# Kernel optimization log

Measured on AMD Instinct MI355X. Metric: run time of the kernel, lower is better.

## Reference

```python
import jax, jax.numpy as jnp
import numpy as np

B, IN, HID, OUT, E, K = 16384, 512, 1024, 512, 16, 4


def setup_inputs() -> dict:
    key = jax.random.key(0)
    k0, k1, k2, k3 = jax.random.split(key, 4)
    return {
        "x": jax.random.normal(k0, (B, IN), jnp.float32),
        "w_gate": jax.random.normal(k1, (IN, E), jnp.float32) * 0.02,
        "w1": jax.random.normal(k2, (E, IN, HID), jnp.float32) * (1.0 / np.sqrt(IN)),
        "b1": jnp.zeros((E, HID), jnp.float32),
        "w2": jax.random.normal(k3, (E, HID, OUT), jnp.float32) * (1.0 / np.sqrt(HID)),
        "b2": jnp.zeros((E, OUT), jnp.float32),
    }


def _top_k_gating(x, w_gate):
    # Eval-mode (no noise) noisy_top_k_gating: logits -> top-(k+1) -> softmax over top-k
    logits = x @ w_gate  # [B, E]
    m = min(K + 1, E)
    top_logits, top_idx = jax.lax.top_k(logits, m)  # [B, m]
    tk_logits = top_logits[:, :K]                    # [B, K]
    tk_idx = top_idx[:, :K]                          # [B, K] int32
    tk_gates = jax.nn.softmax(tk_logits, axis=1)     # softmax over the k selected
    rows = jnp.arange(logits.shape[0])[:, None]
    gates = jnp.zeros_like(logits).at[rows, tk_idx].set(tk_gates)  # sparse [B, E]
    return gates


def reference(x, w_gate, w1, b1, w2, b2):
    # Gating
    gates = _top_k_gating(x, w_gate)  # [B, E], zero for non-selected experts
    # Dispatch/combine: output[b] = sum_e gates[b,e] * MLP_e(x[b]).
    # Torch code only evaluates experts on selected rows; since gates are exactly
    # zero elsewhere, the dense weighted sum below computes identical math.
    y = jnp.zeros((x.shape[0], w2.shape[2]), x.dtype)
    for e in range(E):  # fixed small expert count; each iter is one grouped GEMM pair
        h = jax.nn.relu(x @ w1[e] + b1[e])                 # [B, HID]
        o = jax.nn.softmax(h @ w2[e] + b2[e], axis=1)      # expert MLP ends in Softmax(dim=1)
        y = y + gates[:, e:e + 1] * o
    return y
```

## Files before the change

kernel.cpp:

```cpp
#include <hip/hip_runtime.h>
#include <hip/hip_fp16.h>

typedef _Float16 f16;
typedef _Float16 f16x8 __attribute__((ext_vector_type(8)));
typedef float f32x4 __attribute__((ext_vector_type(4)));

#define MFMA(a,b,c) __builtin_amdgcn_mfma_f32_16x16x32_f16((a),(b),(c),0,0,0)

#define BAR() do { \
  asm volatile("s_waitcnt lgkmcnt(0)" ::: "memory"); \
  __builtin_amdgcn_sched_barrier(0); \
  __builtin_amdgcn_s_barrier(); \
  __builtin_amdgcn_sched_barrier(0); \
} while (0)


__global__ void k_cvt_w1(const float* __restrict__ w1, f16* __restrict__ w1fr) {
  int fid = blockIdx.x * 4 + (threadIdx.x >> 6);
  int l = threadIdx.x & 63;
  int e = fid >> 10, n0 = (fid >> 4) & 63, kc = fid & 15;
  int kbase = kc * 32 + (l >> 4) * 8;
  int col = n0 * 16 + (l & 15);
  const float* src = w1 + ((size_t)e * 512 + kbase) * 1024 + col;
  f16x8 o;
  #pragma unroll
  for (int i = 0; i < 8; i++) o[i] = (f16)src[(size_t)i * 1024];
  *(f16x8*)(w1fr + (size_t)fid * 512 + l * 8) = o;
}

__global__ void k_cvt_w2(const float* __restrict__ w2, f16* __restrict__ w2fr) {
  int fid = blockIdx.x * 4 + (threadIdx.x >> 6);
  int l = threadIdx.x & 63;
  int e = fid >> 10, n0 = (fid >> 5) & 31, kc = fid & 31;
  int kbase = kc * 32 + (l >> 4) * 8;
  int col = n0 * 16 + (l & 15);
  const float* src = w2 + ((size_t)e * 1024 + kbase) * 512 + col;
  f16x8 o;
  #pragma unroll
  for (int i = 0; i < 8; i++) o[i] = (f16)src[(size_t)i * 512];
  *(f16x8*)(w2fr + (size_t)fid * 512 + l * 8) = o;
}

__global__ void k_gate(const float* __restrict__ x, const float* __restrict__ wg,
                       int* __restrict__ tk_idx, float* __restrict__ tk_gate) {
  int w = threadIdx.x >> 6, l = threadIdx.x & 63;
  int r = blockIdx.x * 4 + w;
  float p[16];
  #pragma unroll
  for (int e = 0; e < 16; e++) p[e] = 0.f;
  const float* xr = x + (size_t)r * 512;
  #pragma unroll
  for (int t = 0; t < 8; t++) {
    float xv = xr[t * 64 + l];
    const float* wrow = wg + (t * 64 + l) * 16;
    #pragma unroll
    for (int e = 0; e < 16; e++) p[e] += xv * wrow[e];
  }
  #pragma unroll
  for (int e = 0; e < 16; e++) {
    float v = p[e];
    #pragma unroll
    for (int m = 32; m >= 1; m >>= 1) v += __shfl_xor(v, m);
    p[e] = v;
  }
  unsigned chosen = 0;
  float bv[4]; int bi[4];
  #pragma unroll
  for (int j = 0; j < 4; j++) {
    float best = -3.4e38f; int be = 0;
    #pragma unroll
    for (int e = 0; e < 16; e++) {
      bool ok = !((chosen >> e) & 1u) && (p[e] > best);
      if (ok) { best = p[e]; be = e; }
    }
    chosen |= 1u << be; bv[j] = best; bi[j] = be;
  }
  float m0 = bv[0];
  float e0 = __expf(bv[0] - m0), e1 = __expf(bv[1] - m0),
        e2 = __expf(bv[2] - m0), e3 = __expf(bv[3] - m0);
  float s = e0 + e1 + e2 + e3;
  if (l == 0) {
    *(int4*)(tk_idx + (size_t)r * 4) = make_int4(bi[0], bi[1], bi[2], bi[3]);
    *(float4*)(tk_gate + (size_t)r * 4) = make_float4(e0 / s, e1 / s, e2 / s, e3 / s);
  }
}

__global__ void k_route_count(const int* __restrict__ tk_idx, int* __restrict__ partial) {
  int e = blockIdx.x >> 6, chunk = blockIdx.x & 63;
  int t = threadIdx.x;
  int row = chunk * 256 + t;
  int4 tk = ((const int4*)tk_idx)[row];
  bool match = (tk.x == e) || (tk.y == e) || (tk.z == e) || (tk.w == e);
  unsigned long long m = __ballot(match);
  __shared__ int wc[4];
  if ((t & 63) == 0) wc[t >> 6] = (int)__popcll(m);
  __syncthreads();
  if (t == 0) partial[e * 64 + chunk] = wc[0] + wc[1] + wc[2] + wc[3];
}

__global__ void k_route_scan(const int* __restrict__ partial, int* __restrict__ chunk_base,
                             int* __restrict__ count) {
  int l = threadIdx.x;
  for (int e = 0; e < 16; e++) {
    int v = partial[e * 64 + l];
    int orig = v;
    #pragma unroll
    for (int off = 1; off < 64; off <<= 1) {
      int u = __shfl_up(v, off);
      if (l >= off) v += u;
    }
    chunk_base[e * 64 + l] = v - orig;
    if (l == 63) count[e] = v;
  }
}

__global__ void k_route_scatter(const int* __restrict__ tk_idx, const float* __restrict__ tk_gate,
                                const int* __restrict__ chunk_base, int* __restrict__ rows_pk,
                                float* __restrict__ gates_l) {
  int e = blockIdx.x >> 6, chunk = blockIdx.x & 63;
  int t = threadIdx.x, w = t >> 6, l = t & 63;
  int row = chunk * 256 + t;
  int4 tk = ((const int4*)tk_idx)[row];
  int j = (tk.x == e) ? 0 : (tk.y == e) ? 1 : (tk.z == e) ? 2 : (tk.w == e) ? 3 : -1;
  bool match = (j >= 0);
  unsigned long long m = __ballot(match);
  __shared__ int wc[4];
  if (l == 0) wc[w] = (int)__popcll(m);
  __syncthreads();
  int wbase = 0;
  #pragma unroll
  for (int i = 0; i < 4; i++) if (i < w) wbase += wc[i];
  if (match) {
    int pos = (int)__popcll(m & ((1ULL << l) - 1ULL));
    int idx = e * 16384 + chunk_base[e * 64 + chunk] + wbase + pos;
    rows_pk[idx] = row | (j << 16);
    gates_l[idx] = tk_gate[(size_t)row * 4 + j];
  }
}

__global__ void k_zero(float4* __restrict__ y4) {
  y4[blockIdx.x * 256 + threadIdx.x] = make_float4(0.f, 0.f, 0.f, 0.f);
}

__global__ __launch_bounds__(512, 4) void k_expert(
    const float* __restrict__ x, const f16* __restrict__ w1fr, const f16* __restrict__ w2fr,
    const float* __restrict__ b1, const float* __restrict__ b2,
    const int* __restrict__ count, const int* __restrict__ rows_pk,
    const float* __restrict__ gates_l, float* __restrict__ y)
{
  int p = blockIdx.x;
  int xcd = p & 7, s = p >> 3;
  int e = (xcd << 1) | (s >> 8);
  int rb = s & 255;
  int cnt = count[e];
  int mstart = rb * 64;
  if (mstart >= cnt) return;
  int nvalid = cnt - mstart; if (nvalid > 64) nvalid = 64;

  __shared__ f16 x_lds[2][64 * 136];
  __shared__ f16 h_lds[64 * 264];
  __shared__ int rowarr[64];
  __shared__ float gatearr[64];
  __shared__ float red[2][8][64];

  int t = threadIdx.x, w = t >> 6, l = t & 63;
  int lq = l >> 4, lr = l & 15;

  if (t < 64) {
    int idx = (t < nvalid) ? t : (nvalid - 1);
    int src = e * 16384 + mstart + idx;
    rowarr[t] = rows_pk[src];
    gatearr[t] = gates_l[src];
  }
  BAR();

  int srow = t >> 3, sc0 = (t & 7) * 16;
  const float* sp = x + (size_t)(rowarr[srow] & 0xFFFF) * 512 + sc0;
  char* xl0 = (char*)&x_lds[0][0];
  char* xl1 = (char*)&x_lds[1][0];
  char* hl  = (char*)h_lds;
  int xwb = srow * 272 + sc0 * 2;

  const f16x8* w1f8 = (const f16x8*)w1fr;
  const f16x8* w2f8 = (const f16x8*)w2fr;

  f32x4 acc2[4][4];
  #pragma unroll
  for (int a = 0; a < 4; a++)
    #pragma unroll
    for (int b = 0; b < 4; b++)
      #pragma unroll
      for (int q = 0; q < 4; q++) acc2[a][b][q] = 0.f;

  #pragma unroll 1
  for (int hc = 0; hc < 4; hc++) {
    {
      const float* qp = sp;
      float4 u0 = ((const float4*)qp)[0], u1 = ((const float4*)qp)[1];
      float4 u2 = ((const float4*)qp)[2], u3 = ((const float4*)qp)[3];
      f16x8 v0, v1;
      v0[0]=(f16)u0.x; v0[1]=(f16)u0.y; v0[2]=(f16)u0.z; v0[3]=(f16)u0.w;
      v0[4]=(f16)u1.x; v0[5]=(f16)u1.y; v0[6]=(f16)u1.z; v0[7]=(f16)u1.w;
      v1[0]=(f16)u2.x; v1[1]=(f16)u2.y; v1[2]=(f16)u2.z; v1[3]=(f16)u2.w;
      v1[4]=(f16)u3.x; v1[5]=(f16)u3.y; v1[6]=(f16)u3.z; v1[7]=(f16)u3.w;
      *(f16x8*)(xl0 + xwb) = v0;
      *(f16x8*)(xl0 + xwb + 16) = v1;
    }
    const f16x8* bp1h = w1f8 + ((size_t)((e * 64 + hc * 16 + w * 2) * 16)) * 64 + l;
    f16x8 ba0 = bp1h[0], ba1 = bp1h[16 * 64];
    BAR();

    f32x4 acc1[4][2];
    #pragma unroll
    for (int a = 0; a < 4; a++)
      #pragma unroll
      for (int b = 0; b < 2; b++)
        #pragma unroll
        for (int q = 0; q < 4; q++) acc1[a][b][q] = 0.f;

    #pragma unroll 1
    for (int kk = 0; kk < 4; kk++) {
      char* xbuf = (kk & 1) ? xl1 : xl0;
      char* xnxt = (kk & 1) ? xl0 : xl1;
      float4 u0, u1, u2, u3;
      if (kk < 3) {
        const float* qp = sp + (kk + 1) * 128;
        u0 = ((const float4*)qp)[0]; u1 = ((const float4*)qp)[1];
        u2 = ((const float4*)qp)[2]; u3 = ((const float4*)qp)[3];
      }
      const f16x8* bp1 = bp1h + (size_t)(kk * 4) * 64;
      #pragma unroll
      for (int k4 = 0; k4 < 4; k4++) {
        f16x8 bb0, bb1;
        if (k4 < 3) {
          bb0 = bp1[(k4 + 1) * 64];
          bb1 = bp1[16 * 64 + (k4 + 1) * 64];
        }
        f16x8 av[4];
        #pragma unroll
        for (int mf = 0; mf < 4; mf++)
          av[mf] = *(const f16x8*)(xbuf + (mf * 16 + lr) * 272 + k4 * 64 + lq * 16);
        #pragma unroll
        for (int mf = 0; mf < 4; mf++) {
          acc1[mf][0] = MFMA(av[mf], ba0, acc1[mf][0]);
          acc1[mf][1] = MFMA(av[mf], ba1, acc1[mf][1]);
        }
        if (k4 < 3) { ba0 = bb0; ba1 = bb1; }
      }
      if (kk < 3) {
        f16x8 v0, v1;
        v0[0]=(f16)u0.x; v0[1]=(f16)u0.y; v0[2]=(f16)u0.z; v0[3]=(f16)u0.w;
        v0[4]=(f16)u1.x; v0[5]=(f16)u1.y; v0[6]=(f16)u1.z; v0[7]=(f16)u1.w;
        v1[0]=(f16)u2.x; v1[1]=(f16)u2.y; v1[2]=(f16)u2.z; v1[3]=(f16)u2.w;
        v1[4]=(f16)u3.x; v1[5]=(f16)u3.y; v1[6]=(f16)u3.z; v1[7]=(f16)u3.w;
        *(f16x8*)(xnxt + xwb) = v0;
        *(f16x8*)(xnxt + xwb + 16) = v1;
        const f16x8* bpn = bp1h + (size_t)((kk + 1) * 4) * 64;
        ba0 = bpn[0]; ba1 = bpn[16 * 64];
      }
      BAR();
    }

    #pragma unroll
    for (int nf = 0; nf < 2; nf++) {
      int colc = w * 32 + nf * 16 + lr;
      float bv = b1[e * 1024 + hc * 256 + colc];
      #pragma unroll
      for (int mf = 0; mf < 4; mf++)
        #pragma unroll
        for (int q = 0; q < 4; q++) {
          int row = mf * 16 + lq * 4 + q;
          float hv = fmaxf(acc1[mf][nf][q] + bv, 0.f);
          *(f16*)(hl + row * 528 + colc * 2) = (f16)hv;
        }
    }
    const f16x8* bp2 = w2f8 + ((size_t)((e * 32 + w * 4) * 32 + hc * 8)) * 64 + l;
    f16x8 wa0 = bp2[0], wa1 = bp2[32 * 64], wa2 = bp2[64 * 64], wa3 = bp2[96 * 64];
    BAR();

    #pragma unroll 2
    for (int kc2 = 0; kc2 < 8; kc2++) {
      f16x8 wb0, wb1, wb2, wb3;
      if (kc2 < 7) {
        wb0 = bp2[(kc2 + 1) * 64];
        wb1 = bp2[32 * 64 + (kc2 + 1) * 64];
        wb2 = bp2[64 * 64 + (kc2 + 1) * 64];
        wb3 = bp2[96 * 64 + (kc2 + 1) * 64];
      }
      f16x8 av[4];
      #pragma unroll
      for (int mf = 0; mf < 4; mf++)
        av[mf] = *(const f16x8*)(hl + (mf * 16 + lr) * 528 + kc2 * 64 + lq * 16);
      #pragma unroll
      for (int mf = 0; mf < 4; mf++) {
        acc2[mf][0] = MFMA(av[mf], wa0, acc2[mf][0]);
        acc2[mf][1] = MFMA(av[mf], wa1, acc2[mf][1]);
        acc2[mf][2] = MFMA(av[mf], wa2, acc2[mf][2]);
        acc2[mf][3] = MFMA(av[mf], wa3, acc2[mf][3]);
      }
      if (kc2 < 7) { wa0 = wb0; wa1 = wb1; wa2 = wb2; wa3 = wb3; }
    }
  }

  #pragma unroll
  for (int nf = 0; nf < 4; nf++) {
    float bv = b2[e * 512 + w * 64 + nf * 16 + lr];
    #pragma unroll
    for (int mf = 0; mf < 4; mf++)
      #pragma unroll
      for (int q = 0; q < 4; q++) acc2[mf][nf][q] += bv;
  }

  float rmax[4][4];
  #pragma unroll
  for (int mf = 0; mf < 4; mf++)
    #pragma unroll
    for (int q = 0; q < 4; q++) {
      float v = acc2[mf][0][q];
      #pragma unroll
      for (int nf = 1; nf < 4; nf++) v = fmaxf(v, acc2[mf][nf][q]);
      #pragma unroll
      for (int m = 1; m < 16; m <<= 1) v = fmaxf(v, __shfl_xor(v, m));
      rmax[mf][q] = v;
    }
  if (lr == 0) {
    #pragma unroll
    for (int mf = 0; mf < 4; mf++)
      #pragma unroll
      for (int q = 0; q < 4; q++) red[0][w][mf * 16 + lq * 4 + q] = rmax[mf][q];
  }
  BAR();
  float gmax[4][4];
  #pragma unroll
  for (int mf = 0; mf < 4; mf++)
    #pragma unroll
    for (int q = 0; q < 4; q++) {
      int row = mf * 16 + lq * 4 + q;
      float v = red[0][0][row];
      #pragma unroll
      for (int ww = 1; ww < 8; ww++) v = fmaxf(v, red[0][ww][row]);
      gmax[mf][q] = v;
    }
  float psum[4][4];
  #pragma unroll
  for (int mf = 0; mf < 4; mf++)
    #pragma unroll
    for (int q = 0; q < 4; q++) psum[mf][q] = 0.f;
  #pragma unroll
  for (int mf = 0; mf < 4; mf++)
    #pragma unroll
    for (int nf = 0; nf < 4; nf++)
      #pragma unroll
      for (int q = 0; q < 4; q++) {
        float pp = __expf(acc2[mf][nf][q] - gmax[mf][q]);
        acc2[mf][nf][q] = pp;
        psum[mf][q] += pp;
      }
  #pragma unroll
  for (int mf = 0; mf < 4; mf++)
    #pragma unroll
    for (int q = 0; q < 4; q++) {
      float v = psum[mf][q];
      #pragma unroll
      for (int m = 1; m < 16; m <<= 1) v += __shfl_xor(v, m);
      psum[mf][q] = v;
    }
  if (lr == 0) {
    #pragma unroll
    for (int mf = 0; mf < 4; mf++)
      #pragma unroll
      for (int q = 0; q < 4; q++) red[1][w][mf * 16 + lq * 4 + q] = psum[mf][q];
  }
  BAR();

  #pragma unroll
  for (int mf = 0; mf < 4; mf++) {
    #pragma unroll
    for (int q = 0; q < 4; q++) {
      int row = mf * 16 + lq * 4 + q;
      if (row < nvalid) {
        float ssum = 0.f;
        #pragma unroll
        for (int ww = 0; ww < 8; ww++) ssum += red[1][ww][row];
        float sc = gatearr[row] / ssum;
        int orow = rowarr[row] & 0xFFFF;
        float* yr = y + (size_t)orow * 512 + w * 64 + lr;
        #pragma unroll
        for (int nf = 0; nf < 4; nf++) {
          atomicAdd(yr + nf * 16, acc2[mf][nf][q] * sc);
        }
      }
    }
  }
}

extern "C" void kernel_launch(void* const* d_in, const int* in_sizes, int n_in,
                              void* d_out, int out_size, void* d_ws, size_t ws_size,
                              hipStream_t stream) {
  (void)in_sizes; (void)n_in; (void)out_size; (void)ws_size;
  const float* x  = (const float*)d_in[0];
  const float* wg = (const float*)d_in[1];
  const float* w1 = (const float*)d_in[2];
  const float* b1 = (const float*)d_in[3];
  const float* w2 = (const float*)d_in[4];
  const float* b2 = (const float*)d_in[5];
  float* y = (float*)d_out;

  char* ws = (char*)d_ws;
  size_t off = 0;
  auto alloc = [&](size_t bytes) -> char* {
    char* p = ws + off;
    off += (bytes + 255) & ~(size_t)255;
    return p;
  };
  f16*   w1fr       = (f16*)  alloc((size_t)16 * 512 * 1024 * 2);
  f16*   w2fr       = (f16*)  alloc((size_t)16 * 1024 * 512 * 2);
  int*   tk_idx     = (int*)  alloc((size_t)16384 * 4 * 4);
  float* tk_gate    = (float*)alloc((size_t)16384 * 4 * 4);
  int*   rows_pk    = (int*)  alloc((size_t)16 * 16384 * 4);
  float* gates_l    = (float*)alloc((size_t)16 * 16384 * 4);
  int*   partial    = (int*)  alloc(16 * 64 * 4);
  int*   chunk_base = (int*)  alloc(16 * 64 * 4);
  int*   count      = (int*)  alloc(256);

  k_cvt_w1<<<dim3(4096), dim3(256), 0, stream>>>(w1, w1fr);
  k_cvt_w2<<<dim3(4096), dim3(256), 0, stream>>>(w2, w2fr);
  k_gate<<<dim3(4096), dim3(256), 0, stream>>>(x, wg, tk_idx, tk_gate);
  k_route_count<<<dim3(1024), dim3(256), 0, stream>>>(tk_idx, partial);
  k_route_scan<<<dim3(1), dim3(64), 0, stream>>>(partial, chunk_base, count);
  k_route_scatter<<<dim3(1024), dim3(256), 0, stream>>>(tk_idx, tk_gate, chunk_base,
                                                        rows_pk, gates_l);
  k_zero<<<dim3(8192), dim3(256), 0, stream>>>((float4*)y);
  k_expert<<<dim3(4096), dim3(512), 0, stream>>>(x, w1fr, w2fr, b1, b2,
                                                 count, rows_pk, gates_l, y);
}
```

Before: 450.0 us.

## Double expert block to 16 waves, stage full x tile in swizzled LDS

The expert kernel now uses 1024 threads (16 waves) per block, each wave owning half as many output columns in both GEMMs. The whole 64x512 x tile is loaded and converted to fp16 once into LDS with an XOR swizzle, replacing the per-hc double-buffered reload of x. The h tile also gets an XOR-swizzled layout instead of padding. This removes the repeated x reloads and LDS bank conflicts and adds more waves for latency hiding. In exchange it drops the explicit register prefetch of weights, increases LDS use to about 96KB, which may limit blocks per CU, and doubles the softmax cross-wave reduction width.

Measured after the change: 410.0 us. 8.9% less time.

```diff
diff --git a/kernel.cpp b/kernel.cpp
--- a/kernel.cpp
+++ b/kernel.cpp
@@ -142,7 +142,7 @@
   y4[blockIdx.x * 256 + threadIdx.x] = make_float4(0.f, 0.f, 0.f, 0.f);
 }
 
-__global__ __launch_bounds__(512, 4) void k_expert(
+__global__ __launch_bounds__(1024, 4) void k_expert(
     const float* __restrict__ x, const f16* __restrict__ w1fr, const f16* __restrict__ w2fr,
     const float* __restrict__ b1, const float* __restrict__ b2,
     const int* __restrict__ count, const int* __restrict__ rows_pk,
@@ -157,11 +157,11 @@
   if (mstart >= cnt) return;
   int nvalid = cnt - mstart; if (nvalid > 64) nvalid = 64;
 
-  __shared__ f16 x_lds[2][64 * 136];
-  __shared__ f16 h_lds[64 * 264];
+  __shared__ f16 x_lds[64 * 512];
+  __shared__ f16 h_lds[64 * 256];
   __shared__ int rowarr[64];
   __shared__ float gatearr[64];
-  __shared__ float red[2][8][64];
+  __shared__ float red[2][16][64];
 
   int t = threadIdx.x, w = t >> 6, l = t & 63;
   int lq = l >> 4, lr = l & 15;
@@ -174,137 +174,95 @@
   }
   BAR();
 
-  int srow = t >> 3, sc0 = (t & 7) * 16;
-  const float* sp = x + (size_t)(rowarr[srow] & 0xFFFF) * 512 + sc0;
-  char* xl0 = (char*)&x_lds[0][0];
-  char* xl1 = (char*)&x_lds[1][0];
-  char* hl  = (char*)h_lds;
-  int xwb = srow * 272 + sc0 * 2;
+  {
+    int rX = t >> 4, s0 = t & 15;
+    const float* sp = x + (size_t)(rowarr[rX] & 0xFFFF) * 512;
+    char* xb = (char*)x_lds;
+    #pragma unroll
+    for (int j = 0; j < 4; j++) {
+      int seg = s0 + j * 16;
+      const float* qp = sp + seg * 8;
+      float4 u0 = ((const float4*)qp)[0], u1 = ((const float4*)qp)[1];
+      f16x8 v;
+      v[0]=(f16)u0.x; v[1]=(f16)u0.y; v[2]=(f16)u0.z; v[3]=(f16)u0.w;
+      v[4]=(f16)u1.x; v[5]=(f16)u1.y; v[6]=(f16)u1.z; v[7]=(f16)u1.w;
+      int byte = rX * 1024 + ((seg ^ rX) & 63) * 16;
+      *(f16x8*)(xb + byte) = v;
+    }
+  }
+  BAR();
 
   const f16x8* w1f8 = (const f16x8*)w1fr;
   const f16x8* w2f8 = (const f16x8*)w2fr;
-
-  f32x4 acc2[4][4];
+  char* xb = (char*)x_lds;
+  char* hb = (char*)h_lds;
+
+  f32x4 acc2[4][2];
   #pragma unroll
   for (int a = 0; a < 4; a++)
     #pragma unroll
-    for (int b = 0; b < 4; b++)
+    for (int b = 0; b < 2; b++)
       #pragma unroll
       for (int q = 0; q < 4; q++) acc2[a][b][q] = 0.f;
 
   #pragma unroll 1
   for (int hc = 0; hc < 4; hc++) {
+    f32x4 acc1[4];
+    #pragma unroll
+    for (int a = 0; a < 4; a++)
+      #pragma unroll
+      for (int q = 0; q < 4; q++) acc1[a][q] = 0.f;
+
+    const f16x8* bp1 = w1f8 + ((size_t)((e * 64 + hc * 16 + w) * 16)) * 64 + l;
+    #pragma unroll 4
+    for (int kcg = 0; kcg < 16; kcg++) {
+      f16x8 bf = bp1[kcg * 64];
+      int seg = kcg * 4 + lq;
+      #pragma unroll
+      for (int mf = 0; mf < 4; mf++) {
+        int row = mf * 16 + lr;
+        f16x8 av = *(const f16x8*)(xb + row * 1024 + ((seg ^ row) & 63) * 16);
+        acc1[mf] = MFMA(av, bf, acc1[mf]);
+      }
+    }
+
+    BAR();
     {
-      const float* qp = sp;
-      float4 u0 = ((const float4*)qp)[0], u1 = ((const float4*)qp)[1];
-      float4 u2 = ((const float4*)qp)[2], u3 = ((const float4*)qp)[3];
-      f16x8 v0, v1;
-      v0[0]=(f16)u0.x; v0[1]=(f16)u0.y; v0[2]=(f16)u0.z; v0[3]=(f16)u0.w;
-      v0[4]=(f16)u1.x; v0[5]=(f16)u1.y; v0[6]=(f16)u1.z; v0[7]=(f16)u1.w;
-      v1[0]=(f16)u2.x; v1[1]=(f16)u2.y; v1[2]=(f16)u2.z; v1[3]=(f16)u2.w;
-      v1[4]=(f16)u3.x; v1[5]=(f16)u3.y; v1[6]=(f16)u3.z; v1[7]=(f16)u3.w;
-      *(f16x8*)(xl0 + xwb) = v0;
-      *(f16x8*)(xl0 + xwb + 16) = v1;
-    }
-    const f16x8* bp1h = w1f8 + ((size_t)((e * 64 + hc * 16 + w * 2) * 16)) * 64 + l;
-    f16x8 ba0 = bp1h[0], ba1 = bp1h[16 * 64];
-    BAR();
-
-    f32x4 acc1[4][2];
-    #pragma unroll
-    for (int a = 0; a < 4; a++)
-      #pragma unroll
-      for (int b = 0; b < 2; b++)
-        #pragma unroll
-        for (int q = 0; q < 4; q++) acc1[a][b][q] = 0.f;
-
-    #pragma unroll 1
-    for (int kk = 0; kk < 4; kk++) {
-      char* xbuf = (kk & 1) ? xl1 : xl0;
-      char* xnxt = (kk & 1) ? xl0 : xl1;
-      float4 u0, u1, u2, u3;
-      if (kk < 3) {
-        const float* qp = sp + (kk + 1) * 128;
-        u0 = ((const float4*)qp)[0]; u1 = ((const float4*)qp)[1];
-        u2 = ((const float4*)qp)[2]; u3 = ((const float4*)qp)[3];
-      }
-      const f16x8* bp1 = bp1h + (size_t)(kk * 4) * 64;
-      #pragma unroll
-      for (int k4 = 0; k4 < 4; k4++) {
-        f16x8 bb0, bb1;
-        if (k4 < 3) {
-          bb0 = bp1[(k4 + 1) * 64];
-          bb1 = bp1[16 * 64 + (k4 + 1) * 64];
-        }
-        f16x8 av[4];
-        #pragma unroll
-        for (int mf = 0; mf < 4; mf++)
-          av[mf] = *(const f16x8*)(xbuf + (mf * 16 + lr) * 272 + k4 * 64 + lq * 16);
-        #pragma unroll
-        for (int mf = 0; mf < 4; mf++) {
-          acc1[mf][0] = MFMA(av[mf], ba0, acc1[mf][0]);
-          acc1[mf][1] = MFMA(av[mf], ba1, acc1[mf][1]);
-        }
-        if (k4 < 3) { ba0 = bb0; ba1 = bb1; }
-      }
-      if (kk < 3) {
-        f16x8 v0, v1;
-        v0[0]=(f16)u0.x; v0[1]=(f16)u0.y; v0[2]=(f16)u0.z; v0[3]=(f16)u0.w;
-        v0[4]=(f16)u1.x; v0[5]=(f16)u1.y; v0[6]=(f16)u1.z; v0[7]=(f16)u1.w;
-        v1[0]=(f16)u2.x; v1[1]=(f16)u2.y; v1[2]=(f16)u2.z; v1[3]=(f16)u2.w;
-        v1[4]=(f16)u3.x; v1[5]=(f16)u3.y; v1[6]=(f16)u3.z; v1[7]=(f16)u3.w;
-        *(f16x8*)(xnxt + xwb) = v0;
-        *(f16x8*)(xnxt + xwb + 16) = v1;
-        const f16x8* bpn = bp1h + (size_t)((kk + 1) * 4) * 64;
-        ba0 = bpn[0]; ba1 = bpn[16 * 64];
-      }
-      BAR();
-    }
-
-    #pragma unroll
-    for (int nf = 0; nf < 2; nf++) {
-      int colc = w * 32 + nf * 16 + lr;
-      float bv = b1[e * 1024 + hc * 256 + colc];
+      int cc = w * 16 + lr;
+      float bv = b1[e * 1024 + hc * 256 + cc];
+      int seg = w * 2 + (lr >> 3);
       #pragma unroll
       for (int mf = 0; mf < 4; mf++)
         #pragma unroll
         for (int q = 0; q < 4; q++) {
           int row = mf * 16 + lq * 4 + q;
-          float hv = fmaxf(acc1[mf][nf][q] + bv, 0.f);
-          *(f16*)(hl + row * 528 + colc * 2) = (f16)hv;
+          float hv = fmaxf(acc1[mf][q] + bv, 0.f);
+          int byte = row * 512 + ((seg ^ row) & 31) * 16 + (lr & 7) * 2;
+          *(f16*)(hb + byte) = (f16)hv;
         }
     }
-    const f16x8* bp2 = w2f8 + ((size_t)((e * 32 + w * 4) * 32 + hc * 8)) * 64 + l;
-    f16x8 wa0 = bp2[0], wa1 = bp2[32 * 64], wa2 = bp2[64 * 64], wa3 = bp2[96 * 64];
     BAR();
 
+    const f16x8* bp2a = w2f8 + ((size_t)((e * 32 + w * 2) * 32 + hc * 8)) * 64 + l;
+    const f16x8* bp2b = bp2a + (size_t)32 * 64;
     #pragma unroll 2
     for (int kc2 = 0; kc2 < 8; kc2++) {
-      f16x8 wb0, wb1, wb2, wb3;
-      if (kc2 < 7) {
-        wb0 = bp2[(kc2 + 1) * 64];
-        wb1 = bp2[32 * 64 + (kc2 + 1) * 64];
-        wb2 = bp2[64 * 64 + (kc2 + 1) * 64];
-        wb3 = bp2[96 * 64 + (kc2 + 1) * 64];
+      f16x8 wf0 = bp2a[kc2 * 64];
+      f16x8 wf1 = bp2b[kc2 * 64];
+      int seg = kc2 * 4 + lq;
+      #pragma unroll
+      for (int mf = 0; mf < 4; mf++) {
+        int row = mf * 16 + lr;
+        f16x8 av = *(const f16x8*)(hb + row * 512 + ((seg ^ row) & 31) * 16);
+        acc2[mf][0] = MFMA(av, wf0, acc2[mf][0]);
+        acc2[mf][1] = MFMA(av, wf1, acc2[mf][1]);
       }
-      f16x8 av[4];
-      #pragma unroll
-      for (int mf = 0; mf < 4; mf++)
-        av[mf] = *(const f16x8*)(hl + (mf * 16 + lr) * 528 + kc2 * 64 + lq * 16);
-      #pragma unroll
-      for (int mf = 0; mf < 4; mf++) {
-        acc2[mf][0] = MFMA(av[mf], wa0, acc2[mf][0]);
-        acc2[mf][1] = MFMA(av[mf], wa1, acc2[mf][1]);
-        acc2[mf][2] = MFMA(av[mf], wa2, acc2[mf][2]);
-        acc2[mf][3] = MFMA(av[mf], wa3, acc2[mf][3]);
-      }
-      if (kc2 < 7) { wa0 = wb0; wa1 = wb1; wa2 = wb2; wa3 = wb3; }
-    }
-  }
-
-  #pragma unroll
-  for (int nf = 0; nf < 4; nf++) {
-    float bv = b2[e * 512 + w * 64 + nf * 16 + lr];
+    }
+  }
+
+  #pragma unroll
+  for (int nf = 0; nf < 2; nf++) {
+    float bv = b2[e * 512 + w * 32 + nf * 16 + lr];
     #pragma unroll
     for (int mf = 0; mf < 4; mf++)
       #pragma unroll
@@ -316,9 +274,7 @@
   for (int mf = 0; mf < 4; mf++)
     #pragma unroll
     for (int q = 0; q < 4; q++) {
-      float v = acc2[mf][0][q];
-      #pragma unroll
-      for (int nf = 1; nf < 4; nf++) v = fmaxf(v, acc2[mf][nf][q]);
+      float v = fmaxf(acc2[mf][0][q], acc2[mf][1][q]);
       #pragma unroll
       for (int m = 1; m < 16; m <<= 1) v = fmaxf(v, __shfl_xor(v, m));
       rmax[mf][q] = v;
@@ -338,7 +294,7 @@
       int row = mf * 16 + lq * 4 + q;
       float v = red[0][0][row];
       #pragma unroll
-      for (int ww = 1; ww < 8; ww++) v = fmaxf(v, red[0][ww][row]);
+      for (int ww = 1; ww < 16; ww++) v = fmaxf(v, red[0][ww][row]);
       gmax[mf][q] = v;
     }
   float psum[4][4];
@@ -349,7 +305,7 @@
   #pragma unroll
   for (int mf = 0; mf < 4; mf++)
     #pragma unroll
-    for (int nf = 0; nf < 4; nf++)
+    for (int nf = 0; nf < 2; nf++)
       #pragma unroll
       for (int q = 0; q < 4; q++) {
         float pp = __expf(acc2[mf][nf][q] - gmax[mf][q]);
@@ -381,14 +337,12 @@
       if (row < nvalid) {
         float ssum = 0.f;
         #pragma unroll
-        for (int ww = 0; ww < 8; ww++) ssum += red[1][ww][row];
+        for (int ww = 0; ww < 16; ww++) ssum += red[1][ww][row];
         float sc = gatearr[row] / ssum;
         int orow = rowarr[row] & 0xFFFF;
-        float* yr = y + (size_t)orow * 512 + w * 64 + lr;
-        #pragma unroll
-        for (int nf = 0; nf < 4; nf++) {
-          atomicAdd(yr + nf * 16, acc2[mf][nf][q] * sc);
-        }
+        float* yr = y + (size_t)orow * 512 + w * 32 + lr;
+        atomicAdd(yr, acc2[mf][0][q] * sc);
+        atomicAdd(yr + 16, acc2[mf][1][q] * sc);
       }
     }
   }
@@ -431,6 +385,6 @@
   k_route_scatter<<<dim3(1024), dim3(256), 0, stream>>>(tk_idx, tk_gate, chunk_base,
                                                         rows_pk, gates_l);
   k_zero<<<dim3(8192), dim3(256), 0, stream>>>((float4*)y);
-  k_expert<<<dim3(4096), dim3(512), 0, stream>>>(x, w1fr, w2fr, b1, b2,
-                                                 count, rows_pk, gates_l, y);
-}
+  k_expert<<<dim3(4096), dim3(1024), 0, stream>>>(x, w1fr, w2fr, b1, b2,
+                                                  count, rows_pk, gates_l, y);
+}
```
